# Optimization experiments

Hardware: AMD Instinct MI355X
Metric: run time of the kernel (lower is better)

Reference implementation:

```python
import jax, jax.numpy as jnp
import numpy as np

N, D, EDIM, E, K = 10000, 64, 16, 320000, 16


def _lin(key, o, i):
    # kaiming-normal-ish init, std = sqrt(2/fan_in)
    return jax.random.normal(key, (o, i), dtype=jnp.float32) * (2.0 / i) ** 0.5


def setup_inputs() -> dict:
    key = jax.random.key(0)
    ks = jax.random.split(key, 20)
    inp = {
        "x": jax.random.normal(ks[0], (N, D), dtype=jnp.float32),
        "edge_index": jax.random.randint(ks[1], (2, E), 0, N),
        "edge_attr": jax.random.normal(ks[2], (E, EDIM), dtype=jnp.float32),
        "location_info": jax.random.uniform(ks[3], (N, 4), dtype=jnp.float32),
        "k": K,
    }
    i = 4
    for name in ["sg1", "sg2", "sg3"]:
        inp[name + "_wm"] = _lin(ks[i], D, EDIM + D); i += 1
        inp[name + "_bm"] = jnp.zeros((D,), jnp.float32)
        inp[name + "_wu"] = _lin(ks[i], D, D); i += 1
        inp[name + "_bu"] = jnp.zeros((D,), jnp.float32)
    for name in ["dg1", "dg2"]:
        inp[name + "_w1"] = _lin(ks[i], 2 * D, 2 * D); i += 1
        inp[name + "_b1"] = jnp.zeros((2 * D,), jnp.float32)
        inp[name + "_w2"] = _lin(ks[i], D, 2 * D); i += 1
        inp[name + "_b2"] = jnp.zeros((D,), jnp.float32)
    inp["f1_w"] = _lin(ks[i], D, 5 * D); i += 1
    inp["f1_b"] = jnp.zeros((D,), jnp.float32)
    inp["f2_w"] = _lin(ks[i], D, 6 * D); i += 1
    inp["f2_b"] = jnp.zeros((D,), jnp.float32)
    return inp


def _knn_edges(loc, k, n):
    # dynamic kNN on location_info (euclidean, directed src->dst, with self loops)
    loc = jax.lax.stop_gradient(loc)
    d2 = jnp.sum((loc[:, None, :] - loc[None, :, :]) ** 2, axis=-1)  # [N, N]
    d2 = jnp.where(jnp.eye(n, dtype=bool), jnp.inf, d2)
    _, idx = jax.lax.top_k(-d2, k)               # idx[i] = k nearest sources of target i
    dst = jnp.repeat(jnp.arange(n), k)
    src = idx.reshape(-1)
    loops = jnp.arange(n)
    return jnp.concatenate([src, loops]), jnp.concatenate([dst, loops])


def _forward(x, edge_index, edge_attr, location_info, k,
             sg1_wm, sg1_bm, sg1_wu, sg1_bu,
             sg2_wm, sg2_bm, sg2_wu, sg2_bu,
             sg3_wm, sg3_bm, sg3_wu, sg3_bu,
             dg1_w1, dg1_b1, dg1_w2, dg1_b2,
             dg2_w1, dg2_b1, dg2_w2, dg2_b2,
             f1_w, f1_b, f2_w, f2_b):
    n = x.shape[0]
    relu = jax.nn.relu
    s_src, s_dst = edge_index[0], edge_index[1]  # PyG: row=source j, col=target i

    def static_conv(h, wm, bm, wu, bu):
        m = relu(jnp.concatenate([edge_attr, h[s_src] - h[s_dst]], axis=1) @ wm.T + bm)
        agg = jax.ops.segment_max(m, s_dst, num_segments=n)
        agg = jnp.where(jnp.isfinite(agg), agg, 0.0)  # empty segments -> 0
        return relu(agg @ wu.T + bu)

    d_src, d_dst = _knn_edges(location_info, k, n)

    def dyn_conv(h, w1, b1, w2, b2):
        xi = h[d_dst]
        xj = h[d_src]
        m = relu(relu(jnp.concatenate([xi, xj - xi], axis=1) @ w1.T + b1) @ w2.T + b2)
        return jax.ops.segment_max(m, d_dst, num_segments=n)  # self loops => no empty segments

    h1 = static_conv(x, sg1_wm, sg1_bm, sg1_wu, sg1_bu)
    h2 = static_conv(h1, sg2_wm, sg2_bm, sg2_wu, sg2_bu)
    h3 = static_conv(h2, sg3_wm, sg3_bm, sg3_wu, sg3_bu)
    g1 = dyn_conv(h1, dg1_w1, dg1_b1, dg1_w2, dg1_b2)
    g2 = dyn_conv(g1, dg2_w1, dg2_b1, dg2_w2, dg2_b2)

    cat1 = jnp.concatenate([h1, g1, g2, h2, h3], axis=1)        # [N, 5D]
    fuse1 = relu(cat1 @ f1_w.T + f1_b)                          # [N, D]
    cat2 = jnp.concatenate([fuse1, cat1], axis=1)               # [N, 6D]
    return cat2 @ f2_w.T + f2_b                                 # [N, D]


def reference(x, edge_index, edge_attr, location_info, k,
              sg1_wm, sg1_bm, sg1_wu, sg1_bu,
              sg2_wm, sg2_bm, sg2_wu, sg2_bu,
              sg3_wm, sg3_bm, sg3_wu, sg3_bu,
              dg1_w1, dg1_b1, dg1_w2, dg1_b2,
              dg2_w1, dg2_b1, dg2_w2, dg2_b2,
              f1_w, f1_b, f2_w, f2_b):
    return _forward(x, edge_index, edge_attr, location_info, k,
                    sg1_wm, sg1_bm, sg1_wu, sg1_bu,
                    sg2_wm, sg2_bm, sg2_wu, sg2_bu,
                    sg3_wm, sg3_bm, sg3_wu, sg3_bu,
                    dg1_w1, dg1_b1, dg1_w2, dg1_b2,
                    dg2_w1, dg2_b1, dg2_w2, dg2_b2,
                    f1_w, f1_b, f2_w, f2_b)
```

## Files before the change

kernel.cpp:

```cpp
#include <hip/hip_runtime.h>

#define INF_F __builtin_inff()

typedef __attribute__((ext_vector_type(8))) short short8v;
typedef __attribute__((ext_vector_type(4))) float f32x4;
typedef unsigned long long ull;

__device__ __forceinline__ short f2bf(float x) {
  const unsigned u = __float_as_uint(x);
  return (short)((u + 0x7FFFu + ((u >> 16) & 1u)) >> 16);
}

__device__ __forceinline__ unsigned mbcnt64(ull m) {
  return __builtin_amdgcn_mbcnt_hi((unsigned)(m >> 32),
                                   __builtin_amdgcn_mbcnt_lo((unsigned)m, 0u));
}

#define KNN_G 5
#define KNN_NC (KNN_G*KNN_G*KNN_G*KNN_G)
#define KNN_PCAP 1600

__global__ __launch_bounds__(256) void count2_kernel(
    const float* __restrict__ loc, int* __restrict__ cellcount,
    int* __restrict__ cellid, int n,
    const int* __restrict__ dst, int* __restrict__ deg, int E)
{
  const int i = blockIdx.x * 256 + threadIdx.x;
  if (i < n) {
    const float4 l = *(const float4*)(loc + (size_t)i*4);
    const int cx = min(KNN_G-1, (int)(l.x * (float)KNN_G));
    const int cy = min(KNN_G-1, (int)(l.y * (float)KNN_G));
    const int cz = min(KNN_G-1, (int)(l.z * (float)KNN_G));
    const int cw = min(KNN_G-1, (int)(l.w * (float)KNN_G));
    const int c = ((cx*KNN_G + cy)*KNN_G + cz)*KNN_G + cw;
    cellid[i] = c;
    atomicAdd(&cellcount[c], 1);
  }
  if (i < E) atomicAdd(&deg[dst[i]], 1);
}

__device__ __forceinline__ void scan1b_body(
    const int* __restrict__ in, int* __restrict__ out, int n, int per)
{
  __shared__ int part[1024];
  const int t = threadIdx.x;
  const int lo = t * per, hi = min(lo + per, n);
  int sum = 0;
  for (int idx = lo; idx < hi; ++idx) sum += in[idx];
  int v = sum;
  part[t] = v;
  __syncthreads();
  for (int off = 1; off < 1024; off <<= 1) {
    const int o = (t >= off) ? part[t - off] : 0;
    __syncthreads();
    v += o;
    part[t] = v;
    __syncthreads();
  }
  int run = v - sum;
  for (int idx = lo; idx < hi; ++idx) { out[idx] = run; run += in[idx]; }
  if (t == 1023) out[n] = v;
}

__global__ __launch_bounds__(1024) void scan2_kernel(
    const int* __restrict__ inA, int* __restrict__ outA, int nA, int perA,
    const int* __restrict__ inB, int* __restrict__ outB, int nB, int perB)
{
  if (blockIdx.x == 0) scan1b_body(inA, outA, nA, perA);
  else                 scan1b_body(inB, outB, nB, perB);
}

__global__ __launch_bounds__(256) void scatter2_kernel(
    const float* __restrict__ loc, const int* __restrict__ cellid,
    const int* __restrict__ cellstart, int* __restrict__ cellfill,
    float* __restrict__ locs4s, int* __restrict__ oidx, int n,
    const int* __restrict__ srcs, const int* __restrict__ dsts,
    const int* __restrict__ rowptr, int* __restrict__ dfill,
    int* __restrict__ cs_src, int* __restrict__ cs_eid, int E)
{
  const int i = blockIdx.x * 256 + threadIdx.x;
  if (i < n) {
    const int c = cellid[i];
    const int pos = cellstart[c] + atomicAdd(&cellfill[c], 1);
    *(float4*)(locs4s + (size_t)pos*4) = *(const float4*)(loc + (size_t)i*4);
    oidx[pos] = i;
  }
  if (i < E) {
    const int d = dsts[i];
    const int pos = rowptr[d] + atomicAdd(&dfill[d], 1);
    cs_src[pos] = srcs[i];
    cs_eid[pos] = i;
  }
}

__device__ __forceinline__ ull
knn_refine16(ull* __restrict__ B, int cnt, int lane, ull& topsave)
{
  ull v[5];
#pragma unroll
  for (int s = 0; s < 5; ++s) {
    const int idx = lane + 64*s;
    v[s] = (idx < cnt) ? B[idx] : ~0ull;
  }
  ull tau = ~0ull;
#pragma unroll
  for (int r = 0; r < 16; ++r) {
    ull m = v[0]; int sl = 0;
#pragma unroll
    for (int s = 1; s < 5; ++s) if (v[s] < m) { m = v[s]; sl = s; }
    ull mm = m;
#pragma unroll
    for (int off = 32; off >= 1; off >>= 1) {
      const ull o = __shfl_xor(mm, off, 64);
      if (o < mm) mm = o;
    }
    const bool killer = (m == mm);
#pragma unroll
    for (int s = 0; s < 5; ++s) if (killer && sl == s) v[s] = ~0ull;
    if (lane == r) topsave = mm;
    tau = mm;
  }
  if (lane < 16) B[lane] = topsave;
  return tau;
}

__device__ __forceinline__ int
knn_filter(ull* __restrict__ B, int cnt, int lane, ull& tau)
{
  ull v[5];
#pragma unroll
  for (int s = 0; s < 5; ++s) {
    const int idx = lane + 64*s;
    v[s] = (idx < cnt) ? B[idx] : ~0ull;
  }
  ull g = v[0];
#pragma unroll
  for (int s = 1; s < 5; ++s) if (v[s] < g) g = v[s];
  { ull o = __shfl_xor(g, 1, 64); if (o < g) g = o;
    o = __shfl_xor(g, 2, 64); if (o < g) g = o; }
  ull t = g;
#pragma unroll
  for (int off = 4; off <= 32; off <<= 1) {
    const ull o = __shfl_xor(t, off, 64);
    if (o > t) t = o;
  }
  int nc = 0;
#pragma unroll
  for (int s = 0; s < 5; ++s) {
    const bool keep = (v[s] <= t) && (v[s] != ~0ull);
    const ull mask = __ballot(keep);
    if (mask) {
      const unsigned pre = mbcnt64(mask);
      if (keep) B[nc + pre] = v[s];
      nc += (int)__popcll(mask);
    }
  }
  tau = t;
  return nc;
}

__device__ void knn_body(int blk, ull* __restrict__ Bs, int* __restrict__ PosAll,
                         const float* __restrict__ locs4s,
                         const int* __restrict__ oidx,
                         const int* __restrict__ cellstart,
                         int* __restrict__ knn, int n)
{
#pragma clang fp contract(off)
  constexpr int TRIG = 256;
  const int wave = threadIdx.x >> 6, lane = threadIdx.x & 63;
  const int t = blk * 4 + wave;
  if (t >= n) return;
  ull* B = Bs + wave * 320;
  int* Pos = PosAll + wave * KNN_PCAP;

  const float4 L = *(const float4*)(locs4s + (size_t)t*4);
  const float tx = L.x, ty = L.y, tz = L.z, tw = L.w;
  const int cx = min(KNN_G-1, (int)(tx * (float)KNN_G));
  const int cy = min(KNN_G-1, (int)(ty * (float)KNN_G));
  const int cz = min(KNN_G-1, (int)(tz * (float)KNN_G));
  const int cw = min(KNN_G-1, (int)(tw * (float)KNN_G));

  ull tau = ~0ull;
  ull topsave = ~0ull;
  int cnt = 0;

  auto boundB = [&](int mr) -> float {
    const float w = 1.0f / (float)KNN_G;
    float Bv = INF_F;
    if (cx - mr >= 1)         Bv = fminf(Bv, tx - (float)(cx - mr) * w);
    if (cx + mr <= KNN_G - 2) Bv = fminf(Bv, (float)(cx + mr + 1) * w - tx);
    if (cy - mr >= 1)         Bv = fminf(Bv, ty - (float)(cy - mr) * w);
    if (cy + mr <= KNN_G - 2) Bv = fminf(Bv, (float)(cy + mr + 1) * w - ty);
    if (cz - mr >= 1)         Bv = fminf(Bv, tz - (float)(cz - mr) * w);
    if (cz + mr <= KNN_G - 2) Bv = fminf(Bv, (float)(cz + mr + 1) * w - tz);
    if (cw - mr >= 1)         Bv = fminf(Bv, tw - (float)(cw - mr) * w);
    if (cw + mr <= KNN_G - 2) Bv = fminf(Bv, (float)(cw + mr + 1) * w - tw);
    return Bv;
  };

  auto do_range = [&](int ps, int pe) {
    for (int p0 = ps; p0 < pe; p0 += 64) {
      const int p = p0 + lane;
      ull key = ~0ull;
      if (p < pe && p != t) {
        const float4 q = *(const float4*)(locs4s + (size_t)p*4);
        const int oj = oidx[p];
        const float a0 = q.x - tx, a1 = q.y - ty, a2 = q.z - tz, a3 = q.w - tw;
        const float s0 = a0*a0, s1 = a1*a1, s2 = a2*a2, s3 = a3*a3;
        const float d = ((s0 + s1) + s2) + s3;
        key = ((ull)__float_as_uint(d) << 32) | (unsigned)oj;
      }
      const bool surv = key < tau;
      const ull mask = __ballot(surv);
      if (mask) {
        const unsigned pre = mbcnt64(mask);
        if (surv) B[cnt + pre] = key;
        cnt += (int)__popcll(mask);
        if (cnt > TRIG) cnt = knn_filter(B, cnt, lane, tau);
      }
    }
  };

  int psv = 0, pev = 0;
  if (lane < 27) {
    const int cr = (lane == 0) ? 13 : (lane <= 13 ? lane - 1 : lane);
    const int ax = cx + (cr / 9) - 1;
    const int ay = cy + ((cr / 3) % 3) - 1;
    const int az = cz + (cr % 3) - 1;
    if (ax >= 0 && ax < KNN_G && ay >= 0 && ay < KNN_G &&
        az >= 0 && az < KNN_G) {
      const int base = ((ax*KNN_G + ay)*KNN_G + az)*KNN_G;
      const int wlo = max(cw-1, 0), whi = min(cw+1, KNN_G-1);
      psv = cellstart[base + wlo];
      pev = cellstart[base + whi + 1];
    }
  }
  const int len = max(pev - psv, 0);
  int cum = len;
#pragma unroll
  for (int off = 1; off < 64; off <<= 1) {
    const int o = __shfl_up(cum, off, 64);
    if (lane >= off) cum += o;
  }
  const int T = __shfl(cum, 63, 64);
  const int startv = cum - len;

  for (int p = psv, f = startv; p < pev && f < KNN_PCAP; ++p, ++f) Pos[f] = p;

  const int Tb = min(T, KNN_PCAP);
  const int Tm1b = Tb - 1;
  float4 qn; int ojn = 0, pgn = 0; bool vn = false;
  {
    vn = lane < Tb;
    pgn = Pos[min(lane, Tm1b)];
    qn = *(const float4*)(locs4s + (size_t)pgn*4);
    ojn = oidx[pgn];
  }
  for (int f0 = 0; f0 < Tb; f0 += 64) {
    const float4 qc = qn; const int ojc = ojn, pgc = pgn; const bool vc = vn;
    const int fN = f0 + 64 + lane;
    vn = fN < Tb;
    if (f0 + 64 < Tb) {
      pgn = Pos[min(fN, Tm1b)];
      qn = *(const float4*)(locs4s + (size_t)pgn*4);
      ojn = oidx[pgn];
    }
    ull key = ~0ull;
    if (vc && pgc != t) {
      const float a0 = qc.x - tx, a1 = qc.y - ty, a2 = qc.z - tz, a3 = qc.w - tw;
      const float s0 = a0*a0, s1 = a1*a1, s2 = a2*a2, s3 = a3*a3;
      const float d = ((s0 + s1) + s2) + s3;
      key = ((ull)__float_as_uint(d) << 32) | (unsigned)ojc;
    }
    const bool surv = key < tau;
    const ull mask = __ballot(surv);
    if (mask) {
      const unsigned pre = mbcnt64(mask);
      if (surv) B[cnt + pre] = key;
      cnt += (int)__popcll(mask);
      if (cnt > TRIG) cnt = knn_filter(B, cnt, lane, tau);
    }
  }
  if (T > KNN_PCAP) {
    for (int r = 0; r < 27; ++r) {
      const int st = __shfl(startv, r, 64);
      const int ps = __shfl(psv, r, 64);
      const int pe = __shfl(pev, r, 64);
      const int done = min(max(KNN_PCAP - st, 0), pe - ps);
      if (ps + done < pe) do_range(ps + done, pe);
    }
  }

  for (int m = 2; m <= KNN_G - 1; ++m) {
    if (cnt > 16) { tau = knn_refine16(B, cnt, lane, topsave); cnt = 16; }
    if (tau != ~0ull) {
      const float taud = __uint_as_float((unsigned)(tau >> 32));
      const float Bv = boundB(m - 1);
      if (Bv == INF_F || taud < Bv * Bv * 0.99999f) break;
    }
    const int xlo = max(cx-m, 0), xhi = min(cx+m, KNN_G-1);
    for (int ax = xlo; ax <= xhi; ++ax) {
      const bool xe = (ax == cx-m) || (ax == cx+m);
      const int ylo = max(cy-m, 0), yhi = min(cy+m, KNN_G-1);
      for (int ay = ylo; ay <= yhi; ++ay) {
        const bool ye = (ay == cy-m) || (ay == cy+m);
        const int zlo = max(cz-m, 0), zhi = min(cz+m, KNN_G-1);
        for (int az = zlo; az <= zhi; ++az) {
          const bool ze = (az == cz-m) || (az == cz+m);
          const int base = ((ax*KNN_G + ay)*KNN_G + az)*KNN_G;
          if (xe | ye | ze) {
            const int wlo = max(cw-m, 0), whi = min(cw+m, KNN_G-1);
            do_range(cellstart[base+wlo], cellstart[base+whi+1]);
          } else {
            if (cw-m >= 0) {
              const int c = base + cw - m;
              do_range(cellstart[c], cellstart[c+1]);
            }
            if (cw+m <= KNN_G-1) {
              const int c = base + cw + m;
              do_range(cellstart[c], cellstart[c+1]);
            }
          }
        }
      }
    }
  }
  (void)knn_refine16(B, cnt, lane, topsave);
  const int i = oidx[t];
  if (lane < 16) knn[(size_t)i*16 + lane] = (int)(topsave & 0xFFFFFFFFull);
}

__global__ __launch_bounds__(256) void mega_kernel(
    const float* __restrict__ locs4s, const int* __restrict__ oidx,
    const int* __restrict__ cellstart, int* __restrict__ knn, int n,
    const float* __restrict__ ea, const int* __restrict__ cs_eid,
    float* __restrict__ eac, int E,
    const float* __restrict__ w1A, const float* __restrict__ b1A,
    float* __restrict__ wpqA, float* __restrict__ bpqA,
    const float* __restrict__ w1B, const float* __restrict__ b1B,
    float* __restrict__ wpqB, float* __restrict__ bpqB,
    int KB, int EB)
{
  __shared__ ull Bs[4 * 320];
  __shared__ int Pos[4 * KNN_PCAP];
  const int bid = blockIdx.x;
  if (bid < KB) {
    knn_body(bid, Bs, Pos, locs4s, oidx, cellstart, knn, n);
  } else if (bid < KB + EB) {
    const int idx = (bid - KB) * 256 + threadIdx.x;
    if (idx < E * 4) {
      const int p = idx >> 2, c = idx & 3;
      *(float4*)(eac + (size_t)p*16 + c*4) =
          *(const float4*)(ea + (size_t)cs_eid[p]*16 + c*4);
    }
  } else {
    const int gidx = (bid - KB - EB) * 256 + threadIdx.x;
    const int l = gidx >> 13;
    const int idx = gidx & 8191;
    const float* w1 = l ? w1B : w1A;
    const float* b1 = l ? b1B : b1A;
    float* wpq = l ? wpqB : wpqA;
    float* bpq = l ? bpqB : bpqA;
    const int o = idx >> 6, i = idx & 63;
    const float a = w1[o*128 + i], b = w1[o*128 + 64 + i];
    wpq[idx] = a - b;
    wpq[128*64 + idx] = b;
    if (idx < 128) { bpq[idx] = b1[idx]; bpq[128 + idx] = 0.f; }
  }
}

__global__ __launch_bounds__(256) void static_msg_kernel(
    const float* __restrict__ R, const float* __restrict__ eac,
    const float* __restrict__ wm, const float* __restrict__ bm,
    const int* __restrict__ cs_src, const int* __restrict__ rowptr,
    float* __restrict__ agg, int n)
{
  const int wave = threadIdx.x >> 6, lane = threadIdx.x & 63;
  const int d = blockIdx.x * 4 + wave;
  if (d >= n) return;
  const int beg = rowptr[d], end = rowptr[d+1];
  const int deg = end - beg;
  const int grp = lane >> 4, li = lane & 15;

  short8v bfr[4];
#pragma unroll
  for (int nt = 0; nt < 4; ++nt) {
    short8v b = (short8v)0;
    if (grp < 2) {
      const int ch = nt*16 + li;
#pragma unroll
      for (int j = 0; j < 8; ++j) b[j] = f2bf(wm[ch*80 + grp*8 + j]);
    }
    bfr[nt] = b;
  }
  float basev[4];
#pragma unroll
  for (int nt = 0; nt < 4; ++nt) {
    const int ch = nt*16 + li;
    basev[nt] = bm[ch] - R[(size_t)d*64 + ch];
  }

  float vmax[4] = {0.f, 0.f, 0.f, 0.f};
  const f32x4 zero = (f32x4)0.f;
  for (int m0 = 0; m0 < deg; m0 += 16) {
    short8v a = (short8v)0;
    const int erow = m0 + li;
    if (grp < 2 && erow < deg) {
      const float4* ep = (const float4*)(eac + (size_t)(beg + erow)*16 + grp*8);
      const float4 q0 = ep[0], q1 = ep[1];
      a[0]=f2bf(q0.x); a[1]=f2bf(q0.y); a[2]=f2bf(q0.z); a[3]=f2bf(q0.w);
      a[4]=f2bf(q1.x); a[5]=f2bf(q1.y); a[6]=f2bf(q1.z); a[7]=f2bf(q1.w);
    }
    f32x4 Dv[4];
#pragma unroll
    for (int nt = 0; nt < 4; ++nt)
      Dv[nt] = __builtin_amdgcn_mfma_f32_16x16x32_bf16(a, bfr[nt], zero, 0, 0, 0);
#pragma unroll
    for (int j = 0; j < 4; ++j) {
      const int m = m0 + grp*4 + j;
      if (m < deg) {
        const int s = cs_src[beg + m];
        const float* Rs = R + (size_t)s*64;
#pragma unroll
        for (int nt = 0; nt < 4; ++nt) {
          const float acc = Dv[nt][j] + Rs[nt*16 + li] + basev[nt];
          vmax[nt] = fmaxf(vmax[nt], fmaxf(acc, 0.f));
        }
      }
    }
  }
#pragma unroll
  for (int nt = 0; nt < 4; ++nt) {
    float m = vmax[nt];
    m = fmaxf(m, __shfl_xor(m, 16, 64));
    m = fmaxf(m, __shfl_xor(m, 32, 64));
    vmax[nt] = m;
  }
  float r = vmax[0];
  r = (grp == 1) ? vmax[1] : r;
  r = (grp == 2) ? vmax[2] : r;
  r = (grp == 3) ? vmax[3] : r;
  agg[(size_t)d*64 + lane] = r;
}

template<bool RELU, bool ACC>
__global__ __launch_bounds__(256) void linear_kernel(
    const float* __restrict__ A, int lda,
    const float* __restrict__ W, int ldw,
    const float* __restrict__ bias,
    float* __restrict__ C, int ldc, int M, int K)
{
  __shared__ short As[64 * 72];
  __shared__ short Ws[64 * 72];
  const int tid = threadIdx.x;
  const int wave = tid >> 6, lane = tid & 63;
  const int grp = lane >> 4, li = lane & 15;
  const int m0 = blockIdx.x * 64;
  const int c0 = blockIdx.y * 64;

  f32x4 acc[4];
#pragma unroll
  for (int nt = 0; nt < 4; ++nt) acc[nt] = (f32x4)0.f;

  const int srow = tid >> 2;
  const int sc16 = (tid & 3) * 16;

  for (int kt = 0; kt < K; kt += 64) {
    {
      short tmp[16];
      const int gr = m0 + srow;
      if (gr < M) {
        const float* ar = A + (size_t)gr*lda + kt + sc16;
#pragma unroll
        for (int u = 0; u < 4; ++u) {
          const float4 v = *(const float4*)(ar + u*4);
          tmp[u*4+0] = f2bf(v.x); tmp[u*4+1] = f2bf(v.y);
          tmp[u*4+2] = f2bf(v.z); tmp[u*4+3] = f2bf(v.w);
        }
      } else {
#pragma unroll
        for (int u = 0; u < 16; ++u) tmp[u] = 0;
      }
      *(short8v*)&As[srow*72 + sc16]     = *(short8v*)&tmp[0];
      *(short8v*)&As[srow*72 + sc16 + 8] = *(short8v*)&tmp[8];
      const float* wr = W + (size_t)(c0 + srow)*ldw + kt + sc16;
#pragma unroll
      for (int u = 0; u < 4; ++u) {
        const float4 v = *(const float4*)(wr + u*4);
        tmp[u*4+0] = f2bf(v.x); tmp[u*4+1] = f2bf(v.y);
        tmp[u*4+2] = f2bf(v.z); tmp[u*4+3] = f2bf(v.w);
      }
      *(short8v*)&Ws[srow*72 + sc16]     = *(short8v*)&tmp[0];
      *(short8v*)&Ws[srow*72 + sc16 + 8] = *(short8v*)&tmp[8];
    }
    __syncthreads();
#pragma unroll
    for (int ks = 0; ks < 2; ++ks) {
      const short8v a = *(const short8v*)&As[(wave*16 + li)*72 + ks*32 + grp*8];
#pragma unroll
      for (int nt = 0; nt < 4; ++nt) {
        const short8v b = *(const short8v*)&Ws[(nt*16 + li)*72 + ks*32 + grp*8];
        acc[nt] = __builtin_amdgcn_mfma_f32_16x16x32_bf16(a, b, acc[nt], 0, 0, 0);
      }
    }
    __syncthreads();
  }

#pragma unroll
  for (int nt = 0; nt < 4; ++nt) {
    const int ch = c0 + nt*16 + li;
    const float b = bias ? bias[ch] : 0.f;
#pragma unroll
    for (int j = 0; j < 4; ++j) {
      const int gr = m0 + wave*16 + grp*4 + j;
      if (gr < M) {
        float v = acc[nt][j] + b;
        if (RELU) v = fmaxf(v, 0.f);
        float* cp = C + (size_t)gr*ldc + ch;
        if (ACC) v += *cp;
        *cp = v;
      }
    }
  }
}

#define TPW 4

__global__ __launch_bounds__(256) void dyn_mfma_kernel(
    const float* __restrict__ PQ,
    const float* __restrict__ W2, const float* __restrict__ b2,
    const int* __restrict__ knn, float* __restrict__ out, int ldo, int n)
{
  __shared__ short w2s[64 * 136];
  __shared__ short Ts[4][17 * 136];
  const int tid = threadIdx.x;
  const int wave = tid >> 6, lane = tid & 63;

  for (int idx = tid; idx < 64 * 128; idx += 256) {
    const int c = idx >> 7, k = idx & 127;
    w2s[c*136 + k] = f2bf(W2[c*128 + k]);
  }
  __syncthreads();

  short8v bfr[4][4];
#pragma unroll
  for (int nt = 0; nt < 4; ++nt)
#pragma unroll
    for (int kt = 0; kt < 4; ++kt)
      bfr[nt][kt] = *(const short8v*)&w2s[(nt*16 + (lane&15))*136 +
                                          kt*32 + (lane>>4)*8];
  const float b2v = b2[lane];
  short* T = Ts[wave];

  for (int tg = 0; tg < TPW; ++tg) {
    const int i = (blockIdx.x * 4 + wave) * TPW + tg;
    if (i >= n) break;
    const size_t i16 = (size_t)i * 16;

    for (int s = 0; s < 9; ++s) {
      const int slot = lane + 64*s;
      if (slot < 544) {
        const int row = slot >> 5, k4 = slot & 31;
        const int j = (row < 16) ? knn[i16 + row] : i;
        const float4 p = *(const float4*)(PQ + (size_t)i*256 + k4*4);
        const float4 q = *(const float4*)(PQ + (size_t)j*256 + 128 + k4*4);
        const float t0 = fmaxf(p.x + q.x, 0.f), t1 = fmaxf(p.y + q.y, 0.f);
        const float t2 = fmaxf(p.z + q.z, 0.f), t3 = fmaxf(p.w + q.w, 0.f);
        int2 w;
        w.x = ((int)(unsigned short)f2bf(t1) << 16) | (unsigned short)f2bf(t0);
        w.y = ((int)(unsigned short)f2bf(t3) << 16) | (unsigned short)f2bf(t2);
        *(int2*)&T[row*136 + k4*4] = w;
      }
    }

    f32x4 acc0[4], acc1[4];
#pragma unroll
    for (int nt = 0; nt < 4; ++nt) {
      acc0[nt] = (f32x4)0.f;
      acc1[nt] = (f32x4)0.f;
    }
#pragma unroll
    for (int kt = 0; kt < 4; ++kt) {
      const short8v a1 = *(const short8v*)&T[(lane&15)*136 + kt*32 + (lane>>4)*8];
      const short8v a2 = *(const short8v*)&T[16*136 + kt*32 + (lane>>4)*8];
#pragma unroll
      for (int nt = 0; nt < 4; ++nt) {
        acc0[nt] = __builtin_amdgcn_mfma_f32_16x16x32_bf16(a1, bfr[nt][kt], acc0[nt], 0, 0, 0);
        acc1[nt] = __builtin_amdgcn_mfma_f32_16x16x32_bf16(a2, bfr[nt][kt], acc1[nt], 0, 0, 0);
      }
    }

    float v[4];
#pragma unroll
    for (int nt = 0; nt < 4; ++nt) {
      float m = fmaxf(fmaxf(acc0[nt][0], acc0[nt][1]),
                      fmaxf(acc0[nt][2], acc0[nt][3]));
      m = fmaxf(m, acc1[nt][0]);
      m = fmaxf(m, __shfl_xor(m, 16, 64));
      m = fmaxf(m, __shfl_xor(m, 32, 64));
      v[nt] = m;
    }
    const int g = lane >> 4;
    float r = v[0];
    r = (g == 1) ? v[1] : r;
    r = (g == 2) ? v[2] : r;
    r = (g == 3) ? v[3] : r;
    out[(size_t)i*ldo + lane] = fmaxf(r + b2v, 0.f);
  }
}

extern "C" void kernel_launch(void* const* d_in, const int* in_sizes, int n_in,
                              void* d_out, int out_size, void* d_ws, size_t ws_size,
                              hipStream_t stream)
{
  const float* x   = (const float*)d_in[0];
  const int*   ei  = (const int*)d_in[1];
  const float* ea  = (const float*)d_in[2];
  const float* loc = (const float*)d_in[3];
  const float* sg_wm[3] = {(const float*)d_in[5],  (const float*)d_in[9],  (const float*)d_in[13]};
  const float* sg_bm[3] = {(const float*)d_in[6],  (const float*)d_in[10], (const float*)d_in[14]};
  const float* sg_wu[3] = {(const float*)d_in[7],  (const float*)d_in[11], (const float*)d_in[15]};
  const float* sg_bu[3] = {(const float*)d_in[8],  (const float*)d_in[12], (const float*)d_in[16]};
  const float* dg_w1[2] = {(const float*)d_in[17], (const float*)d_in[21]};
  const float* dg_b1[2] = {(const float*)d_in[18], (const float*)d_in[22]};
  const float* dg_w2[2] = {(const float*)d_in[19], (const float*)d_in[23]};
  const float* dg_b2[2] = {(const float*)d_in[20], (const float*)d_in[24]};
  const float* f1_w = (const float*)d_in[25];
  const float* f1_b = (const float*)d_in[26];
  const float* f2_w = (const float*)d_in[27];
  const float* f2_b = (const float*)d_in[28];
  float* out = (float*)d_out;

  const int n    = in_sizes[0] / 64;
  const int Etot = in_sizes[1] / 2;
  const int* srcp = ei;
  const int* dstp = ei + Etot;

  char* basep = (char*)d_ws;
  size_t cur = 0;
  auto alloc = [&](size_t bytes) -> void* {
    void* p = basep + cur;
    cur = (cur + bytes + 255) & ~(size_t)255;
    return p;
  };
  float* CAT  = (float*)alloc((size_t)n * 320 * 4);
  float* Rb   = (float*)alloc((size_t)n * 64 * 4);
  float* PQb  = (float*)alloc((size_t)n * 256 * 4);
  float* agg  = (float*)alloc((size_t)n * 64 * 4);
  float* fu1  = (float*)alloc((size_t)n * 64 * 4);
  float* wpq[2];
  float* bpq[2];
  wpq[0] = (float*)alloc(256 * 64 * 4);  bpq[0] = (float*)alloc(256 * 4);
  wpq[1] = (float*)alloc(256 * 64 * 4);  bpq[1] = (float*)alloc(256 * 4);
  int* knnb   = (int*)alloc((size_t)n * 16 * 4);
  int* zeros     = (int*)alloc((size_t)(2*KNN_NC + 2*n) * 4);
  int* cellcount = zeros;
  int* cellfill  = zeros + KNN_NC;
  int* deg       = zeros + 2*KNN_NC;
  int* dfill     = zeros + 2*KNN_NC + n;
  int* cellstart = (int*)alloc((size_t)(KNN_NC + 1) * 4);
  int* cellidb   = (int*)alloc((size_t)n * 4);
  float* locs4s  = (float*)alloc((size_t)n * 4 * 4);
  int* oidx      = (int*)alloc((size_t)n * 4);
  int* rowptr    = (int*)alloc((size_t)(n + 1) * 4);
  int* cs_src    = (int*)alloc((size_t)Etot * 4);
  int* cs_eid    = (int*)alloc((size_t)Etot * 4);
  float* ea_csr  = (float*)alloc((size_t)Etot * 16 * 4);
  (void)ws_size; (void)n_in; (void)out_size;

  const int nbE = (Etot + 255) / 256;

  hipMemsetAsync(zeros, 0, (size_t)(2*KNN_NC + 2*n) * 4, stream);
  count2_kernel<<<nbE, 256, 0, stream>>>(loc, cellcount, cellidb, n,
                                         dstp, deg, Etot);
  scan2_kernel<<<2, 1024, 0, stream>>>(cellcount, cellstart, KNN_NC,
                                       (KNN_NC + 1023) / 1024,
                                       deg, rowptr, n, (n + 1023) / 1024);
  scatter2_kernel<<<nbE, 256, 0, stream>>>(loc, cellidb, cellstart, cellfill,
                                           locs4s, oidx, n,
                                           srcp, dstp, rowptr, dfill,
                                           cs_src, cs_eid, Etot);
  const int KB = (n + 3) / 4;
  const int EB = (Etot * 4 + 255) / 256;
  mega_kernel<<<KB + EB + 64, 256, 0, stream>>>(
      locs4s, oidx, cellstart, knnb, n,
      ea, cs_eid, ea_csr, Etot,
      dg_w1[0], dg_b1[0], wpq[0], bpq[0],
      dg_w1[1], dg_b1[1], wpq[1], bpq[1],
      KB, EB);

  const int mb = (n + 63) / 64;
  auto lin = [&](const float* A, int lda, const float* W, int ldw, const float* bias,
                 float* C, int ldc, int K, int ncols, bool relu, bool accum) {
    dim3 grid(mb, ncols / 64);
    if (relu)       linear_kernel<true,  false><<<grid, 256, 0, stream>>>(A, lda, W, ldw, bias, C, ldc, n, K);
    else if (accum) linear_kernel<false, true ><<<grid, 256, 0, stream>>>(A, lda, W, ldw, bias, C, ldc, n, K);
    else            linear_kernel<false, false><<<grid, 256, 0, stream>>>(A, lda, W, ldw, bias, C, ldc, n, K);
  };

  const float* hin = x; int hlda = 64;
  float* hout[3] = {CAT + 0, CAT + 192, CAT + 256};
  for (int l = 0; l < 3; ++l) {
    lin(hin, hlda, sg_wm[l] + 16, 80, nullptr, Rb, 64, 64, 64, false, false);
    static_msg_kernel<<<(n + 3) / 4, 256, 0, stream>>>(Rb, ea_csr, sg_wm[l],
                                                       sg_bm[l], cs_src,
                                                       rowptr, agg, n);
    lin(agg, 64, sg_wu[l], 64, sg_bu[l], hout[l], 320, 64, 64, true, false);
    hin = hout[l]; hlda = 320;
  }

  const float* din[2] = {CAT + 0, CAT + 64};
  float* doutp[2] = {CAT + 64, CAT + 128};
  const int db = (n + 4*TPW - 1) / (4*TPW);
  for (int l = 0; l < 2; ++l) {
    lin(din[l], 320, wpq[l], 64, bpq[l], PQb, 256, 64, 256, false, false);
    dyn_mfma_kernel<<<db, 256, 0, stream>>>(PQb, dg_w2[l], dg_b2[l],
                                            knnb, doutp[l], 320, n);
  }

  lin(CAT, 320, f1_w, 320, f1_b, fu1, 64, 320, 64, true,  false);
  lin(CAT, 320, f2_w + 64, 384, f2_b, out, 64, 320, 64, false, false);
  lin(fu1, 64, f2_w, 384, nullptr, out, 64, 64, 64, false, true);
}
```

Baseline: 336.0 us.

## Fuse static-conv update with next layer's message GEMM and merge fusion head

```diff
diff --git a/kernel.cpp b/kernel.cpp
--- a/kernel.cpp
+++ b/kernel.cpp
@@ -443,6 +443,26 @@
   agg[(size_t)d*64 + lane] = r;
 }
 
+__device__ __forceinline__ void stage_tile_bf16(
+    short* __restrict__ S, const float* __restrict__ src, int srow, int sc16,
+    bool valid)
+{
+  short tmp[16];
+  if (valid) {
+#pragma unroll
+    for (int u = 0; u < 4; ++u) {
+      const float4 v = *(const float4*)(src + u*4);
+      tmp[u*4+0] = f2bf(v.x); tmp[u*4+1] = f2bf(v.y);
+      tmp[u*4+2] = f2bf(v.z); tmp[u*4+3] = f2bf(v.w);
+    }
+  } else {
+#pragma unroll
+    for (int u = 0; u < 16; ++u) tmp[u] = 0;
+  }
+  *(short8v*)&S[srow*72 + sc16]     = *(short8v*)&tmp[0];
+  *(short8v*)&S[srow*72 + sc16 + 8] = *(short8v*)&tmp[8];
+}
+
 template<bool RELU, bool ACC>
 __global__ __launch_bounds__(256) void linear_kernel(
     const float* __restrict__ A, int lda,
@@ -466,33 +486,9 @@
   const int sc16 = (tid & 3) * 16;
 
   for (int kt = 0; kt < K; kt += 64) {
-    {
-      short tmp[16];
-      const int gr = m0 + srow;
-      if (gr < M) {
-        const float* ar = A + (size_t)gr*lda + kt + sc16;
-#pragma unroll
-        for (int u = 0; u < 4; ++u) {
-          const float4 v = *(const float4*)(ar + u*4);
-          tmp[u*4+0] = f2bf(v.x); tmp[u*4+1] = f2bf(v.y);
-          tmp[u*4+2] = f2bf(v.z); tmp[u*4+3] = f2bf(v.w);
-        }
-      } else {
-#pragma unroll
-        for (int u = 0; u < 16; ++u) tmp[u] = 0;
-      }
-      *(short8v*)&As[srow*72 + sc16]     = *(short8v*)&tmp[0];
-      *(short8v*)&As[srow*72 + sc16 + 8] = *(short8v*)&tmp[8];
-      const float* wr = W + (size_t)(c0 + srow)*ldw + kt + sc16;
-#pragma unroll
-      for (int u = 0; u < 4; ++u) {
-        const float4 v = *(const float4*)(wr + u*4);
-        tmp[u*4+0] = f2bf(v.x); tmp[u*4+1] = f2bf(v.y);
-        tmp[u*4+2] = f2bf(v.z); tmp[u*4+3] = f2bf(v.w);
-      }
-      *(short8v*)&Ws[srow*72 + sc16]     = *(short8v*)&tmp[0];
-      *(short8v*)&Ws[srow*72 + sc16 + 8] = *(short8v*)&tmp[8];
-    }
+    const int gr = m0 + srow;
+    stage_tile_bf16(As, A + (size_t)gr*lda + kt + sc16, srow, sc16, gr < M);
+    stage_tile_bf16(Ws, W + (size_t)(c0 + srow)*ldw + kt + sc16, srow, sc16, true);
     __syncthreads();
 #pragma unroll
     for (int ks = 0; ks < 2; ++ks) {
@@ -520,6 +516,155 @@
         if (ACC) v += *cp;
         *cp = v;
       }
+    }
+  }
+}
+
+__global__ __launch_bounds__(256) void fused_hR_kernel(
+    const float* __restrict__ A,
+    const float* __restrict__ Wu, const float* __restrict__ bu,
+    float* __restrict__ Hout, int ldh,
+    const float* __restrict__ Wm,
+    float* __restrict__ Rout, int M)
+{
+  __shared__ short As[64 * 72];
+  __shared__ short Ws[64 * 72];
+  const int tid = threadIdx.x;
+  const int wave = tid >> 6, lane = tid & 63;
+  const int grp = lane >> 4, li = lane & 15;
+  const int m0 = blockIdx.x * 64;
+  const int srow = tid >> 2;
+  const int sc16 = (tid & 3) * 16;
+
+  {
+    const int gr = m0 + srow;
+    stage_tile_bf16(As, A + (size_t)gr*64 + sc16, srow, sc16, gr < M);
+    stage_tile_bf16(Ws, Wu + (size_t)srow*64 + sc16, srow, sc16, true);
+  }
+  __syncthreads();
+  f32x4 acc[4];
+#pragma unroll
+  for (int nt = 0; nt < 4; ++nt) acc[nt] = (f32x4)0.f;
+#pragma unroll
+  for (int ks = 0; ks < 2; ++ks) {
+    const short8v a = *(const short8v*)&As[(wave*16 + li)*72 + ks*32 + grp*8];
+#pragma unroll
+    for (int nt = 0; nt < 4; ++nt) {
+      const short8v b = *(const short8v*)&Ws[(nt*16 + li)*72 + ks*32 + grp*8];
+      acc[nt] = __builtin_amdgcn_mfma_f32_16x16x32_bf16(a, b, acc[nt], 0, 0, 0);
+    }
+  }
+  __syncthreads();
+
+  stage_tile_bf16(Ws, Wm + (size_t)srow*80 + sc16, srow, sc16, true);
+#pragma unroll
+  for (int nt = 0; nt < 4; ++nt) {
+    const int ch = nt*16 + li;
+    const float b = bu[ch];
+#pragma unroll
+    for (int j = 0; j < 4; ++j) {
+      const int row = wave*16 + grp*4 + j;
+      const int gr = m0 + row;
+      const float v = fmaxf(acc[nt][j] + b, 0.f);
+      if (gr < M) Hout[(size_t)gr*ldh + ch] = v;
+      As[row*72 + ch] = f2bf(v);
+    }
+  }
+  __syncthreads();
+
+  f32x4 acc2[4];
+#pragma unroll
+  for (int nt = 0; nt < 4; ++nt) acc2[nt] = (f32x4)0.f;
+#pragma unroll
+  for (int ks = 0; ks < 2; ++ks) {
+    const short8v a = *(const short8v*)&As[(wave*16 + li)*72 + ks*32 + grp*8];
+#pragma unroll
+    for (int nt = 0; nt < 4; ++nt) {
+      const short8v b = *(const short8v*)&Ws[(nt*16 + li)*72 + ks*32 + grp*8];
+      acc2[nt] = __builtin_amdgcn_mfma_f32_16x16x32_bf16(a, b, acc2[nt], 0, 0, 0);
+    }
+  }
+#pragma unroll
+  for (int nt = 0; nt < 4; ++nt) {
+    const int ch = nt*16 + li;
+#pragma unroll
+    for (int j = 0; j < 4; ++j) {
+      const int gr = m0 + wave*16 + grp*4 + j;
+      if (gr < M) Rout[(size_t)gr*64 + ch] = acc2[nt][j];
+    }
+  }
+}
+
+__global__ __launch_bounds__(256) void fusion_kernel(
+    const float* __restrict__ CAT,
+    const float* __restrict__ f1w, const float* __restrict__ f1b,
+    const float* __restrict__ f2w, const float* __restrict__ f2bias,
+    float* __restrict__ out, int M)
+{
+  __shared__ short As[64 * 72];
+  __shared__ short W1s[64 * 72];
+  __shared__ short W2s[64 * 72];
+  const int tid = threadIdx.x;
+  const int wave = tid >> 6, lane = tid & 63;
+  const int grp = lane >> 4, li = lane & 15;
+  const int m0 = blockIdx.x * 64;
+  const int srow = tid >> 2;
+  const int sc16 = (tid & 3) * 16;
+
+  f32x4 acc1[4], acc2[4];
+#pragma unroll
+  for (int nt = 0; nt < 4; ++nt) { acc1[nt] = (f32x4)0.f; acc2[nt] = (f32x4)0.f; }
+
+  for (int kt = 0; kt < 320; kt += 64) {
+    const int gr = m0 + srow;
+    stage_tile_bf16(As,  CAT + (size_t)gr*320 + kt + sc16, srow, sc16, gr < M);
+    stage_tile_bf16(W1s, f1w + (size_t)srow*320 + kt + sc16, srow, sc16, true);
+    stage_tile_bf16(W2s, f2w + (size_t)srow*384 + 64 + kt + sc16, srow, sc16, true);
+    __syncthreads();
+#pragma unroll
+    for (int ks = 0; ks < 2; ++ks) {
+      const short8v a = *(const short8v*)&As[(wave*16 + li)*72 + ks*32 + grp*8];
+#pragma unroll
+      for (int nt = 0; nt < 4; ++nt) {
+        const short8v b1 = *(const short8v*)&W1s[(nt*16 + li)*72 + ks*32 + grp*8];
+        const short8v b2 = *(const short8v*)&W2s[(nt*16 + li)*72 + ks*32 + grp*8];
+        acc1[nt] = __builtin_amdgcn_mfma_f32_16x16x32_bf16(a, b1, acc1[nt], 0, 0, 0);
+        acc2[nt] = __builtin_amdgcn_mfma_f32_16x16x32_bf16(a, b2, acc2[nt], 0, 0, 0);
+      }
+    }
+    __syncthreads();
+  }
+
+  stage_tile_bf16(W1s, f2w + (size_t)srow*384 + sc16, srow, sc16, true);
+#pragma unroll
+  for (int nt = 0; nt < 4; ++nt) {
+    const int ch = nt*16 + li;
+    const float b = f1b[ch];
+#pragma unroll
+    for (int j = 0; j < 4; ++j) {
+      const int row = wave*16 + grp*4 + j;
+      const float v = fmaxf(acc1[nt][j] + b, 0.f);
+      As[row*72 + ch] = f2bf(v);
+    }
+  }
+  __syncthreads();
+#pragma unroll
+  for (int ks = 0; ks < 2; ++ks) {
+    const short8v a = *(const short8v*)&As[(wave*16 + li)*72 + ks*32 + grp*8];
+#pragma unroll
+    for (int nt = 0; nt < 4; ++nt) {
+      const short8v b = *(const short8v*)&W1s[(nt*16 + li)*72 + ks*32 + grp*8];
+      acc2[nt] = __builtin_amdgcn_mfma_f32_16x16x32_bf16(a, b, acc2[nt], 0, 0, 0);
+    }
+  }
+#pragma unroll
+  for (int nt = 0; nt < 4; ++nt) {
+    const int ch = nt*16 + li;
+    const float b = f2bias[ch];
+#pragma unroll
+    for (int j = 0; j < 4; ++j) {
+      const int gr = m0 + wave*16 + grp*4 + j;
+      if (gr < M) out[(size_t)gr*64 + ch] = acc2[nt][j] + b;
     }
   }
 }
@@ -647,7 +792,6 @@
   float* Rb   = (float*)alloc((size_t)n * 64 * 4);
   float* PQb  = (float*)alloc((size_t)n * 256 * 4);
   float* agg  = (float*)alloc((size_t)n * 64 * 4);
-  float* fu1  = (float*)alloc((size_t)n * 64 * 4);
   float* wpq[2];
   float* bpq[2];
   wpq[0] = (float*)alloc(256 * 64 * 4);  bpq[0] = (float*)alloc(256 * 4);
@@ -691,34 +835,38 @@
 
   const int mb = (n + 63) / 64;
   auto lin = [&](const float* A, int lda, const float* W, int ldw, const float* bias,
-                 float* C, int ldc, int K, int ncols, bool relu, bool accum) {
+                 float* C, int ldc, int K, int ncols, bool relu) {
     dim3 grid(mb, ncols / 64);
-    if (relu)       linear_kernel<true,  false><<<grid, 256, 0, stream>>>(A, lda, W, ldw, bias, C, ldc, n, K);
-    else if (accum) linear_kernel<false, true ><<<grid, 256, 0, stream>>>(A, lda, W, ldw, bias, C, ldc, n, K);
-    else            linear_kernel<false, false><<<grid, 256, 0, stream>>>(A, lda, W, ldw, bias, C, ldc, n, K);
+    if (relu) linear_kernel<true,  false><<<grid, 256, 0, stream>>>(A, lda, W, ldw, bias, C, ldc, n, K);
+    else      linear_kernel<false, false><<<grid, 256, 0, stream>>>(A, lda, W, ldw, bias, C, ldc, n, K);
   };
 
-  const float* hin = x; int hlda = 64;
-  float* hout[3] = {CAT + 0, CAT + 192, CAT + 256};
-  for (int l = 0; l < 3; ++l) {
-    lin(hin, hlda, sg_wm[l] + 16, 80, nullptr, Rb, 64, 64, 64, false, false);
-    static_msg_kernel<<<(n + 3) / 4, 256, 0, stream>>>(Rb, ea_csr, sg_wm[l],
-                                                       sg_bm[l], cs_src,
-                                                       rowptr, agg, n);
-    lin(agg, 64, sg_wu[l], 64, sg_bu[l], hout[l], 320, 64, 64, true, false);
-    hin = hout[l]; hlda = 320;
-  }
+  lin(x, 64, sg_wm[0] + 16, 80, nullptr, Rb, 64, 64, 64, false);
+  static_msg_kernel<<<(n + 3) / 4, 256, 0, stream>>>(Rb, ea_csr, sg_wm[0],
+                                                     sg_bm[0], cs_src,
+                                                     rowptr, agg, n);
+  fused_hR_kernel<<<mb, 256, 0, stream>>>(agg, sg_wu[0], sg_bu[0],
+                                          CAT + 0, 320,
+                                          sg_wm[1] + 16, Rb, n);
+  static_msg_kernel<<<(n + 3) / 4, 256, 0, stream>>>(Rb, ea_csr, sg_wm[1],
+                                                     sg_bm[1], cs_src,
+                                                     rowptr, agg, n);
+  fused_hR_kernel<<<mb, 256, 0, stream>>>(agg, sg_wu[1], sg_bu[1],
+                                          CAT + 192, 320,
+                                          sg_wm[2] + 16, Rb, n);
+  static_msg_kernel<<<(n + 3) / 4, 256, 0, stream>>>(Rb, ea_csr, sg_wm[2],
+                                                     sg_bm[2], cs_src,
+                                                     rowptr, agg, n);
+  lin(agg, 64, sg_wu[2], 64, sg_bu[2], CAT + 256, 320, 64, 64, true);
 
   const float* din[2] = {CAT + 0, CAT + 64};
   float* doutp[2] = {CAT + 64, CAT + 128};
   const int db = (n + 4*TPW - 1) / (4*TPW);
   for (int l = 0; l < 2; ++l) {
-    lin(din[l], 320, wpq[l], 64, bpq[l], PQb, 256, 64, 256, false, false);
+    lin(din[l], 320, wpq[l], 64, bpq[l], PQb, 256, 64, 256, false);
     dyn_mfma_kernel<<<db, 256, 0, stream>>>(PQb, dg_w2[l], dg_b2[l],
                                             knnb, doutp[l], 320, n);
   }
 
-  lin(CAT, 320, f1_w, 320, f1_b, fu1, 64, 320, 64, true,  false);
-  lin(CAT, 320, f2_w + 64, 384, f2_b, out, 64, 320, 64, false, false);
-  lin(fu1, 64, f2_w, 384, nullptr, out, 64, 64, 64, false, true);
-}
+  fusion_kernel<<<mb, 256, 0, stream>>>(CAT, f1_w, f1_b, f2_w, f2_b, out, n);
+}
```

New measurement: 312.8 us. -6.9%, faster.
